# Kernel tuning notes

Measured on AMD Instinct MI355X. Metric: run time of the kernel, lower is better.

Reference implementation:

```python
import jax, jax.numpy as jnp
import numpy as np

N_FEAT = 512
N_HEAD = 8
CONTEXT_SIZES = (31, 61)
HEADS_PER_SCALE = N_HEAD // len(CONTEXT_SIZES)  # 4
B, T = 4, 2048


def _windows(v, cs):
    """Gather overlapping local windows (faithful to chunkwise with N_c=1).
    v: [B, T, D] -> [B, T, cs, D], zero-padded at both ends by (cs-1)//2."""
    Bv, Tv, D = v.shape
    half = (cs - 1) // 2
    vp = jnp.pad(v, ((0, 0), (half, half), (0, 0)))
    idx = jnp.arange(Tv)[:, None] + jnp.arange(cs)[None, :]  # [T, cs]
    return vp[:, idx, :]


def setup_inputs() -> dict:
    key0 = jax.random.key(0)
    ks = jax.random.split(key0, 12)
    s = 0.02
    inp = {
        "query": jax.random.normal(ks[0], (B, T, N_FEAT), jnp.float32),
        "key": jax.random.normal(ks[1], (B, T, N_FEAT), jnp.float32),
        "value": jax.random.normal(ks[2], (B, T, N_FEAT), jnp.float32),
        # Linear weights stored torch-style [out_features, in_features]
        "w1_0": jax.random.normal(ks[3], (N_FEAT, N_FEAT), jnp.float32) * s,
        "w1_1": jax.random.normal(ks[4], (N_FEAT, N_FEAT), jnp.float32) * s,
        "w2_0": jax.random.normal(ks[5], (HEADS_PER_SCALE * CONTEXT_SIZES[0], N_FEAT), jnp.float32) * s,
        "w2_1": jax.random.normal(ks[6], (HEADS_PER_SCALE * CONTEXT_SIZES[1], N_FEAT), jnp.float32) * s,
        "w3_0": jax.random.normal(ks[7], (N_FEAT, N_FEAT), jnp.float32) * s,
        "w3_1": jax.random.normal(ks[8], (N_FEAT, N_FEAT), jnp.float32) * s,
        "scale_weights": jnp.ones((len(CONTEXT_SIZES),), jnp.float32) / len(CONTEXT_SIZES),
        "w_out": jax.random.normal(ks[9], (N_FEAT, N_FEAT), jnp.float32) * s,
    }
    return inp


def reference(query, key, value, w1_0, w1_1, w2_0, w2_1, w3_0, w3_1, scale_weights, w_out):
    # key is unused by the original module's forward.
    Bq, Tq, Fq = query.shape
    hd = Fq // N_HEAD  # per-head dim within a scale after splitting n_feat by heads_per_scale? No:
    head_dim = Fq // HEADS_PER_SCALE  # matches original: D // heads_per_scale
    outs = []
    for (w1, w2, w3, cs) in ((w1_0, w2_0, w3_0, CONTEXT_SIZES[0]),
                             (w1_1, w2_1, w3_1, CONTEXT_SIZES[1])):
        q = query @ w1.T                      # [B,T,F]
        v = value @ w3.T                      # [B,T,F]
        logits = jax.nn.relu(q) @ w2.T        # [B,T,HS*cs]
        attn = jax.nn.softmax(logits.reshape(Bq, Tq, HEADS_PER_SCALE, cs), axis=-1)
        # local windows of v: [B,T,cs,F] -> [B,T,cs,HS,head_dim]
        vw = _windows(v, cs).reshape(Bq, Tq, cs, HEADS_PER_SCALE, head_dim)
        x = jnp.einsum('bthc,btchd->bthd', attn, vw).reshape(Bq, Tq, Fq)
        outs.append(x)
    sw = jax.nn.softmax(scale_weights)
    x = sw[0] * outs[0] + sw[1] * outs[1]
    return x @ w_out.T
```

## Files before the change

### kernel.cpp

```cpp
#include <hip/hip_runtime.h>

typedef unsigned short u16;
typedef unsigned long long u64;
typedef float floatx4 __attribute__((ext_vector_type(4)));
typedef short shortx8 __attribute__((ext_vector_type(8)));

__device__ inline u16 f2bf(float f) {
  unsigned u = __float_as_uint(f);
  u += 0x7fffu + ((u >> 16) & 1u);
  return (u16)(u >> 16);
}
__device__ inline float bflo(unsigned u) { return __uint_as_float(u << 16); }
__device__ inline float bfhi(unsigned u) { return __uint_as_float(u & 0xffff0000u); }

__device__ __forceinline__ void gl16(const u16* g, const u16* l) {
  __builtin_amdgcn_global_load_lds(
      (const __attribute__((address_space(1))) unsigned int*)(u64)(const void*)g,
      (__attribute__((address_space(3))) unsigned int*)(unsigned)(u64)(const void*)l,
      16, 0, 0);
}

__global__ __launch_bounds__(256) void convert_all(
    const float* __restrict__ q, const float* __restrict__ v,
    const float* __restrict__ w10, const float* __restrict__ w11,
    const float* __restrict__ w30, const float* __restrict__ w31,
    const float* __restrict__ wo, const float* __restrict__ w20,
    const float* __restrict__ w21, u16* __restrict__ base) {
  size_t e = ((size_t)blockIdx.x * 256 + threadIdx.x) * 4;
  const float* src;
  u16* dst;
  size_t le;
  unsigned prows;
  if (e < 4194304ull)      { src = q;   dst = base;            le = e;            prows = 0x7fffffffu; }
  else if (e < 8388608ull) { src = v;   dst = base + 4194304;  le = e - 4194304;  prows = 0x7fffffffu; }
  else if (e < 8650752ull) { src = w10; dst = base + 8388608;  le = e - 8388608;  prows = 0x7fffffffu; }
  else if (e < 8912896ull) { src = w11; dst = base + 8650752;  le = e - 8650752;  prows = 0x7fffffffu; }
  else if (e < 9175040ull) { src = w30; dst = base + 8912896;  le = e - 8912896;  prows = 0x7fffffffu; }
  else if (e < 9437184ull) { src = w31; dst = base + 9175040;  le = e - 9175040;  prows = 0x7fffffffu; }
  else if (e < 9699328ull) { src = wo;  dst = base + 9437184;  le = e - 9437184;  prows = 0x7fffffffu; }
  else if (e < 9764864ull) { src = w20; dst = base + 9699328;  le = e - 9699328;  prows = 124; }
  else                     { src = w21; dst = base + 9764864;  le = e - 9764864;  prows = 244; }
  float4 val = make_float4(0.f, 0.f, 0.f, 0.f);
  if ((unsigned)(le >> 9) < prows) val = *(const float4*)(src + le);
  unsigned p0 = (unsigned)f2bf(val.x) | ((unsigned)f2bf(val.y) << 16);
  unsigned p1 = (unsigned)f2bf(val.z) | ((unsigned)f2bf(val.w) << 16);
  *(uint2*)(dst + le) = make_uint2(p0, p1);
}

template <int OUTBF>
__device__ __forceinline__ void gemm_core(
    const u16* __restrict__ A, int lda, const u16* __restrict__ W, int ldw,
    float* __restrict__ Cf, u16* __restrict__ Cb, int ldc, int relu,
    u16* lA, u16* lB) {
  const int tid = threadIdx.x;
  const int wave = tid >> 6, lane = tid & 63;
  const int wm = (wave >> 1) * 64, wn = (wave & 1) * 64;
  const int lr = lane & 15, kq = (lane >> 4) * 8;
  const int sr = lane >> 2, sc = (lane & 3) * 8;

  floatx4 acc[4][4];
#pragma unroll
  for (int i = 0; i < 4; ++i)
#pragma unroll
    for (int j = 0; j < 4; ++j) acc[i][j] = (floatx4){0.f, 0.f, 0.f, 0.f};

  const u16* ga0 = A + (u64)(wave * 32 + sr) * lda + sc;
  const u16* ga1 = A + (u64)(wave * 32 + 16 + sr) * lda + sc;
  const u16* gb0 = W + (u64)(wave * 32 + sr) * ldw + sc;
  const u16* gb1 = W + (u64)(wave * 32 + 16 + sr) * ldw + sc;
  u16* la0 = lA + (wave * 32) * 32;
  u16* la1 = lA + (wave * 32 + 16) * 32;
  u16* lb0 = lB + (wave * 32) * 32;
  u16* lb1 = lB + (wave * 32 + 16) * 32;

  for (int k0 = 0; k0 < 512; k0 += 32) {
    __syncthreads();
    gl16(ga0 + k0, la0);
    gl16(ga1 + k0, la1);
    gl16(gb0 + k0, lb0);
    gl16(gb1 + k0, lb1);
    __syncthreads();
    shortx8 af[4], bf8[4];
#pragma unroll
    for (int i = 0; i < 4; ++i) {
      af[i] = *(const shortx8*)&lA[(wm + i * 16 + lr) * 32 + kq];
      bf8[i] = *(const shortx8*)&lB[(wn + i * 16 + lr) * 32 + kq];
    }
#pragma unroll
    for (int mi = 0; mi < 4; ++mi)
#pragma unroll
      for (int ni = 0; ni < 4; ++ni)
        acc[mi][ni] = __builtin_amdgcn_mfma_f32_16x16x32_bf16(af[mi], bf8[ni], acc[mi][ni], 0, 0, 0);
  }
  const int er = wm + (lane >> 4) * 4;
  const int ec = wn + lr;
#pragma unroll
  for (int mi = 0; mi < 4; ++mi)
#pragma unroll
    for (int ni = 0; ni < 4; ++ni)
#pragma unroll
      for (int r = 0; r < 4; ++r) {
        float vv = acc[mi][ni][r];
        if (relu) vv = fmaxf(vv, 0.f);
        u64 off = (u64)(er + mi * 16 + r) * (u64)ldc + (u64)(ec + ni * 16);
        if (OUTBF) Cb[off] = f2bf(vv);
        else Cf[off] = vv;
      }
}

__global__ __launch_bounds__(256, 2) void k_qv(
    const u16* __restrict__ qb, const u16* __restrict__ vb,
    const u16* __restrict__ w1, const u16* __restrict__ w3,
    u16* __restrict__ rq, u16* __restrict__ vc) {
  __shared__ __align__(16) u16 lA[128 * 32];
  __shared__ __align__(16) u16 lB[128 * 32];
  const int bx = blockIdx.x, bn = blockIdx.y * 128;
  const bool isq = bx < 64;
  const int am = (isq ? bx : bx - 64) * 128;
  const u16* A = (isq ? qb : vb) + (u64)am * 512;
  const u16* W = (isq ? w1 : w3) + (u64)bn * 512;
  u16* Cb = (isq ? rq : vc) + (u64)am * 1024 + bn;
  gemm_core<1>(A, 512, W, 512, nullptr, Cb, 1024, isq ? 1 : 0, lA, lB);
}

__global__ __launch_bounds__(256, 2) void k_logits(
    const u16* __restrict__ rq, const u16* __restrict__ w20,
    const u16* __restrict__ w21, float* __restrict__ lg) {
  __shared__ __align__(16) u16 lA[128 * 32];
  __shared__ __align__(16) u16 lB[128 * 32];
  const int am = blockIdx.x * 128;
  const int y = blockIdx.y;
  const u16* A = rq + (u64)am * 1024 + (y == 0 ? 0 : 512);
  const u16* W = (y == 0) ? w20 : (w21 + (u64)(y - 1) * 128 * 512);
  float* Cf = lg + (u64)am * 384 + y * 128;
  gemm_core<0>(A, 1024, W, 512, Cf, nullptr, 384, 0, lA, lB);
}

__global__ __launch_bounds__(256, 2) void k_final(
    const u16* __restrict__ xb, const u16* __restrict__ wo,
    float* __restrict__ out) {
  __shared__ __align__(16) u16 lA[128 * 32];
  __shared__ __align__(16) u16 lB[128 * 32];
  const int am = blockIdx.x * 128, bn = blockIdx.y * 128;
  gemm_core<0>(xb + (u64)am * 512, 512, wo + (u64)bn * 512, 512,
               out + (u64)am * 512 + bn, nullptr, 512, 0, lA, lB);
}

template <int CS>
__device__ __forceinline__ void attn_pass(
    const float* __restrict__ lg, const u16* __restrict__ vbh,
    int bb, int t0, float swv, u16* vl, float* es, float* qsum,
    float* invsum, floatx4 (&accT)[2][4]) {
  constexpr int HALF = (CS - 1) / 2;
  constexpr int SPAN = ((CS + 3) + 3) & ~3;
  constexpr int RV = 64 + SPAN;
  constexpr int VLD = 136;
  const int tid = threadIdx.x;

  __syncthreads();

  for (int i = tid; i < 64 * RV / 4; i += 256)
    ((floatx4*)es)[i] = (floatx4){0.f, 0.f, 0.f, 0.f};
  for (int idx = tid; idx < RV * 16; idx += 256) {
    int r = idx >> 4, d8 = (idx & 15) * 8;
    int t = t0 + r - HALF;
    uint4 u = make_uint4(0u, 0u, 0u, 0u);
    if (r < 64 + CS - 1 && t >= 0 && t < 2048)
      u = *(const uint4*)&vbh[(u64)(bb + t) * 1024 + d8];
    *(uint4*)&vl[r * VLD + d8] = u;
  }
  __syncthreads();

  {
    int tt = tid >> 2, qq = tid & 3;
    float ps = 0.f;
    const float* lrow = lg + (u64)(bb + t0 + tt) * 384;
    for (int c = qq; c < CS; c += 4) {
      float ev = __expf(lrow[c]);
      es[tt * RV + tt + c] = ev;
      ps += ev;
    }
    qsum[tt * 4 + qq] = ps;
  }
  __syncthreads();
  if (tid < 64)
    invsum[tid] = swv / (qsum[tid * 4] + qsum[tid * 4 + 1] +
                         qsum[tid * 4 + 2] + qsum[tid * 4 + 3]);
  __syncthreads();

  const int dg = tid & 31, rg = tid >> 5;
#pragma unroll
  for (int cell = 0; cell < 2; ++cell) {
    int tt0 = (rg + cell * 8) * 4;
    floatx4 acc[4];
#pragma unroll
    for (int i = 0; i < 4; ++i) acc[i] = (floatx4){0.f, 0.f, 0.f, 0.f};
    for (int rb = 0; rb < SPAN; rb += 4) {
      int r = tt0 + rb;
      floatx4 vr[4];
#pragma unroll
      for (int j = 0; j < 4; ++j) {
        uint2 u = *(const uint2*)&vl[(r + j) * VLD + dg * 4];
        vr[j] = (floatx4){bflo(u.x), bfhi(u.x), bflo(u.y), bfhi(u.y)};
      }
#pragma unroll
      for (int i = 0; i < 4; ++i) {
        floatx4 ev = *(const floatx4*)&es[(tt0 + i) * RV + r];
        acc[i] += vr[0] * ev.x;
        acc[i] += vr[1] * ev.y;
        acc[i] += vr[2] * ev.z;
        acc[i] += vr[3] * ev.w;
      }
    }
#pragma unroll
    for (int i = 0; i < 4; ++i)
      accT[cell][i] += acc[i] * invsum[tt0 + i];
  }
}

__global__ __launch_bounds__(256, 1) void k_attn2(
    const float* __restrict__ lg, const u16* __restrict__ vcat,
    const float* __restrict__ swp, u16* __restrict__ xbw) {
  __shared__ __align__(16) float es[64 * 128];
  __shared__ __align__(16) u16 vl[128 * 136];
  __shared__ float qsum[256];
  __shared__ float invsum[64];
  const int tid = threadIdx.x;
  const int t0 = blockIdx.x * 64, h = blockIdx.y, b = blockIdx.z;
  const int bb = b * 2048;
  const int m0 = bb + t0;

  float a0 = swp[0], a1 = swp[1];
  float mx = fmaxf(a0, a1);
  float e0 = __expf(a0 - mx), e1 = __expf(a1 - mx);
  float inv = 1.f / (e0 + e1);

  floatx4 accT[2][4];
#pragma unroll
  for (int c = 0; c < 2; ++c)
#pragma unroll
    for (int i = 0; i < 4; ++i) accT[c][i] = (floatx4){0.f, 0.f, 0.f, 0.f};

  attn_pass<31>(lg + h * 31, vcat + h * 128, bb, t0, e0 * inv,
                vl, es, qsum, invsum, accT);
  attn_pass<61>(lg + 128 + h * 61, vcat + 512 + h * 128, bb, t0, e1 * inv,
                vl, es, qsum, invsum, accT);

  const int dg = tid & 31, rg = tid >> 5;
#pragma unroll
  for (int cell = 0; cell < 2; ++cell)
#pragma unroll
    for (int i = 0; i < 4; ++i) {
      int tt = (rg + cell * 8) * 4 + i;
      floatx4 o = accT[cell][i];
      u64 off = (u64)(m0 + tt) * 512 + (u64)(h * 128 + dg * 4);
      unsigned p0 = (unsigned)f2bf(o.x) | ((unsigned)f2bf(o.y) << 16);
      unsigned p1 = (unsigned)f2bf(o.z) | ((unsigned)f2bf(o.w) << 16);
      *(uint2*)&xbw[off] = make_uint2(p0, p1);
    }
}

extern "C" void kernel_launch(void* const* d_in, const int* in_sizes, int n_in,
                              void* d_out, int out_size, void* d_ws, size_t ws_size,
                              hipStream_t stream) {
  const float* q   = (const float*)d_in[0];
  const float* v   = (const float*)d_in[2];
  const float* w10 = (const float*)d_in[3];
  const float* w11 = (const float*)d_in[4];
  const float* w20 = (const float*)d_in[5];
  const float* w21 = (const float*)d_in[6];
  const float* w30 = (const float*)d_in[7];
  const float* w31 = (const float*)d_in[8];
  const float* sw  = (const float*)d_in[9];
  const float* wo  = (const float*)d_in[10];
  float* out = (float*)d_out;

  u16* base  = (u16*)d_ws;
  u16* qb    = base;
  u16* vb    = base + 4194304;
  u16* w1cat = base + 8388608;
  u16* w3cat = base + 8912896;
  u16* wob   = base + 9437184;
  u16* w2b0  = base + 9699328;
  u16* w2b1  = base + 9764864;
  char* fb = (char*)d_ws + 19791872;
  float* logitsC = (float*)fb;
  u16* rqcat = (u16*)(logitsC + 3145728);
  u16* vcat  = rqcat + 8388608;
  u16* xb    = vcat + 8388608;

  convert_all<<<dim3(9664), dim3(256), 0, stream>>>(q, v, w10, w11, w30, w31, wo, w20, w21, base);

  dim3 blk(256);
  k_qv<<<dim3(128, 8), blk, 0, stream>>>(qb, vb, w1cat, w3cat, rqcat, vcat);
  k_logits<<<dim3(64, 3), blk, 0, stream>>>(rqcat, w2b0, w2b1, logitsC);
  k_attn2<<<dim3(32, 4, 4), blk, 0, stream>>>(logitsC, vcat, sw, xb);
  k_final<<<dim3(64, 4), blk, 0, stream>>>(xb, wob, out);
}
```

Measured before the change: 207.9 us.

## Compute local-window attention with bf16 MFMA on banded prob matrix

Replaces the scalar FMA attention-value accumulation with bf16 MFMA 16x16x32 over a banded, zero-padded exp-logit matrix stored as bf16, with V transposed into LDS. Each wave handles 16 time rows and only iterates over the K blocks its band touches. The output is staged through LDS so global stores are coalesced 16-byte writes. Exp weights now round to bf16 before the matmul while the normaliser stays in fp32, which adds rounding error, and the transpose writes to LDS are scalar 2-byte stores that may cause bank conflicts.

```diff
diff --git a/kernel.cpp b/kernel.cpp
--- a/kernel.cpp
+++ b/kernel.cpp
@@ -10,8 +10,6 @@
   u += 0x7fffu + ((u >> 16) & 1u);
   return (u16)(u >> 16);
 }
-__device__ inline float bflo(unsigned u) { return __uint_as_float(u << 16); }
-__device__ inline float bfhi(unsigned u) { return __uint_as_float(u & 0xffff0000u); }
 
 __device__ __forceinline__ void gl16(const u16* g, const u16* l) {
   __builtin_amdgcn_global_load_lds(
@@ -146,28 +144,38 @@
                out + (u64)am * 512 + bn, nullptr, 512, 0, lA, lB);
 }
 
+#define LDT 152
+
 template <int CS>
-__device__ __forceinline__ void attn_pass(
-    const float* __restrict__ lg, const u16* __restrict__ vbh,
-    int bb, int t0, float swv, u16* vl, float* es, float* qsum,
-    float* invsum, floatx4 (&accT)[2][4]) {
+__device__ __forceinline__ void attn_mfma_pass(
+    const float* __restrict__ lg,
+    const u16* __restrict__ vbh,
+    int bb, int t0, float swv,
+    u16* vT, u16* es16, float* qsum, float* invsum, floatx4 (&o)[8]) {
   constexpr int HALF = (CS - 1) / 2;
-  constexpr int SPAN = ((CS + 3) + 3) & ~3;
-  constexpr int RV = 64 + SPAN;
-  constexpr int VLD = 136;
+  constexpr int NW = 64 + CS - 1;
   const int tid = threadIdx.x;
-
-  __syncthreads();
-
-  for (int i = tid; i < 64 * RV / 4; i += 256)
-    ((floatx4*)es)[i] = (floatx4){0.f, 0.f, 0.f, 0.f};
-  for (int idx = tid; idx < RV * 16; idx += 256) {
-    int r = idx >> 4, d8 = (idx & 15) * 8;
+  const int wave = tid >> 6, lane = tid & 63;
+  const int lr = lane & 15, kq = (lane >> 4) * 8;
+
+  __syncthreads();
+
+  for (int i = tid; i < 64 * LDT / 8; i += 256)
+    ((uint4*)es16)[i] = make_uint4(0u, 0u, 0u, 0u);
+
+#pragma unroll
+  for (int it = 0; it < 8; ++it) {
+    int widx = it * 4 + wave;
+    int rb = (widx >> 4) * 64;
+    int d8 = (widx & 15) * 8;
+    int r = rb + lane;
     int t = t0 + r - HALF;
     uint4 u = make_uint4(0u, 0u, 0u, 0u);
-    if (r < 64 + CS - 1 && t >= 0 && t < 2048)
+    if (r < NW && t >= 0 && t < 2048)
       u = *(const uint4*)&vbh[(u64)(bb + t) * 1024 + d8];
-    *(uint4*)&vl[r * VLD + d8] = u;
+#pragma unroll
+    for (int j = 0; j < 8; ++j)
+      vT[(d8 + j) * LDT + r] = ((const u16*)&u)[j];
   }
   __syncthreads();
 
@@ -177,7 +185,7 @@
     const float* lrow = lg + (u64)(bb + t0 + tt) * 384;
     for (int c = qq; c < CS; c += 4) {
       float ev = __expf(lrow[c]);
-      es[tt * RV + tt + c] = ev;
+      es16[tt * LDT + tt + c] = f2bf(ev);
       ps += ev;
     }
     qsum[tt * 4 + qq] = ps;
@@ -188,44 +196,39 @@
                          qsum[tid * 4 + 2] + qsum[tid * 4 + 3]);
   __syncthreads();
 
-  const int dg = tid & 31, rg = tid >> 5;
-#pragma unroll
-  for (int cell = 0; cell < 2; ++cell) {
-    int tt0 = (rg + cell * 8) * 4;
-    floatx4 acc[4];
-#pragma unroll
-    for (int i = 0; i < 4; ++i) acc[i] = (floatx4){0.f, 0.f, 0.f, 0.f};
-    for (int rb = 0; rb < SPAN; rb += 4) {
-      int r = tt0 + rb;
-      floatx4 vr[4];
-#pragma unroll
-      for (int j = 0; j < 4; ++j) {
-        uint2 u = *(const uint2*)&vl[(r + j) * VLD + dg * 4];
-        vr[j] = (floatx4){bflo(u.x), bfhi(u.x), bflo(u.y), bfhi(u.y)};
-      }
-#pragma unroll
-      for (int i = 0; i < 4; ++i) {
-        floatx4 ev = *(const floatx4*)&es[(tt0 + i) * RV + r];
-        acc[i] += vr[0] * ev.x;
-        acc[i] += vr[1] * ev.y;
-        acc[i] += vr[2] * ev.z;
-        acc[i] += vr[3] * ev.w;
-      }
+  const int kb_lo = (wave * 16) >> 5;
+  const int kb_hi = (wave * 16 + 15 + CS - 1) >> 5;
+  floatx4 acc[8];
+#pragma unroll
+  for (int nt = 0; nt < 8; ++nt) acc[nt] = (floatx4){0.f, 0.f, 0.f, 0.f};
+  for (int kb = kb_lo; kb <= kb_hi; ++kb) {
+    shortx8 af = *(const shortx8*)&es16[(wave * 16 + lr) * LDT + kb * 32 + kq];
+#pragma unroll
+    for (int nt = 0; nt < 8; ++nt) {
+      shortx8 bf8 = *(const shortx8*)&vT[(nt * 16 + lr) * LDT + kb * 32 + kq];
+      acc[nt] = __builtin_amdgcn_mfma_f32_16x16x32_bf16(af, bf8, acc[nt], 0, 0, 0);
     }
-#pragma unroll
-    for (int i = 0; i < 4; ++i)
-      accT[cell][i] += acc[i] * invsum[tt0 + i];
-  }
-}
-
-__global__ __launch_bounds__(256, 1) void k_attn2(
+  }
+  float invs[4];
+#pragma unroll
+  for (int rr = 0; rr < 4; ++rr)
+    invs[rr] = invsum[wave * 16 + (lane >> 4) * 4 + rr];
+#pragma unroll
+  for (int nt = 0; nt < 8; ++nt)
+#pragma unroll
+    for (int rr = 0; rr < 4; ++rr) o[nt][rr] += acc[nt][rr] * invs[rr];
+}
+
+__global__ __launch_bounds__(256, 1) void k_attn3(
     const float* __restrict__ lg, const u16* __restrict__ vcat,
     const float* __restrict__ swp, u16* __restrict__ xbw) {
-  __shared__ __align__(16) float es[64 * 128];
-  __shared__ __align__(16) u16 vl[128 * 136];
+  __shared__ __align__(16) u16 vT[128 * LDT];
+  __shared__ __align__(16) u16 es16[64 * LDT];
   __shared__ float qsum[256];
   __shared__ float invsum[64];
   const int tid = threadIdx.x;
+  const int wave = tid >> 6, lane = tid & 63;
+  const int lr = lane & 15;
   const int t0 = blockIdx.x * 64, h = blockIdx.y, b = blockIdx.z;
   const int bb = b * 2048;
   const int m0 = bb + t0;
@@ -235,29 +238,32 @@
   float e0 = __expf(a0 - mx), e1 = __expf(a1 - mx);
   float inv = 1.f / (e0 + e1);
 
-  floatx4 accT[2][4];
-#pragma unroll
-  for (int c = 0; c < 2; ++c)
-#pragma unroll
-    for (int i = 0; i < 4; ++i) accT[c][i] = (floatx4){0.f, 0.f, 0.f, 0.f};
-
-  attn_pass<31>(lg + h * 31, vcat + h * 128, bb, t0, e0 * inv,
-                vl, es, qsum, invsum, accT);
-  attn_pass<61>(lg + 128 + h * 61, vcat + 512 + h * 128, bb, t0, e1 * inv,
-                vl, es, qsum, invsum, accT);
-
-  const int dg = tid & 31, rg = tid >> 5;
-#pragma unroll
-  for (int cell = 0; cell < 2; ++cell)
-#pragma unroll
-    for (int i = 0; i < 4; ++i) {
-      int tt = (rg + cell * 8) * 4 + i;
-      floatx4 o = accT[cell][i];
-      u64 off = (u64)(m0 + tt) * 512 + (u64)(h * 128 + dg * 4);
-      unsigned p0 = (unsigned)f2bf(o.x) | ((unsigned)f2bf(o.y) << 16);
-      unsigned p1 = (unsigned)f2bf(o.z) | ((unsigned)f2bf(o.w) << 16);
-      *(uint2*)&xbw[off] = make_uint2(p0, p1);
+  floatx4 o[8];
+#pragma unroll
+  for (int nt = 0; nt < 8; ++nt) o[nt] = (floatx4){0.f, 0.f, 0.f, 0.f};
+
+  attn_mfma_pass<31>(lg + h * 31, vcat + h * 128, bb, t0, e0 * inv,
+                     vT, es16, qsum, invsum, o);
+  attn_mfma_pass<61>(lg + 128 + h * 61, vcat + 512 + h * 128, bb, t0, e1 * inv,
+                     vT, es16, qsum, invsum, o);
+
+  __syncthreads();
+#pragma unroll
+  for (int nt = 0; nt < 8; ++nt)
+#pragma unroll
+    for (int rr = 0; rr < 4; ++rr) {
+      int trow = wave * 16 + (lane >> 4) * 4 + rr;
+      es16[trow * LDT + nt * 16 + lr] = f2bf(o[nt][rr]);
     }
+  __syncthreads();
+#pragma unroll
+  for (int rep = 0; rep < 4; ++rep) {
+    int idx = rep * 256 + tid;
+    int trow = idx >> 4;
+    int col8 = (idx & 15) * 8;
+    uint4 u = *(const uint4*)&es16[trow * LDT + col8];
+    *(uint4*)&xbw[(u64)(m0 + trow) * 512 + h * 128 + col8] = u;
+  }
 }
 
 extern "C" void kernel_launch(void* const* d_in, const int* in_sizes, int n_in,
@@ -294,6 +300,6 @@
   dim3 blk(256);
   k_qv<<<dim3(128, 8), blk, 0, stream>>>(qb, vb, w1cat, w3cat, rqcat, vcat);
   k_logits<<<dim3(64, 3), blk, 0, stream>>>(rqcat, w2b0, w2b1, logitsC);
-  k_attn2<<<dim3(32, 4, 4), blk, 0, stream>>>(logitsC, vcat, sw, xb);
+  k_attn3<<<dim3(32, 4, 4), blk, 0, stream>>>(logitsC, vcat, sw, xb);
   k_final<<<dim3(64, 4), blk, 0, stream>>>(xb, wob, out);
 }
```

Result: faster. 174.3 us (-16.2%).
